# Kernel tuning notes

Hardware: AMD Instinct MI355X
Metric: run time of the kernel (lower is better)

The kernel has to match this reference:

```python
import jax, jax.numpy as jnp
import numpy as np

ALPHA = 0.85  # position gain (init kwarg alpha)
BETA = 0.005  # velocity gain (init kwarg beta)


def setup_inputs() -> dict:
    key = jax.random.key(0)
    Z = jax.random.normal(key, (4096, 8192), dtype=jnp.float32)
    return {"Z": Z}


def reference(Z) -> jnp.ndarray:
    # alpha-beta (g-h) filter recurrence, scanned over the time axis.
    #   diff = z - p;  x = p + a*diff;  v += b*diff;  p = x + v
    # Initial state: p = Z[:, 0], v = 0  (so x_0 == Z[:, 0]).
    a = jnp.asarray(ALPHA, Z.dtype)
    b = jnp.asarray(BETA, Z.dtype)

    def step(carry, z):
        p, v = carry
        diff = z - p
        x = p + a * diff
        v = v + b * diff
        p = x + v
        return (p, v), x

    p0 = Z[:, 0]
    v0 = jnp.zeros_like(p0)
    # scan over time: Z.T has shape [T, B]
    _, xs = jax.lax.scan(step, (p0, v0), Z.T)
    return xs.T  # [B, T]
```

## Files before the change

kernel.cpp:

```cpp
#include <hip/hip_runtime.h>


#define A_CONST 0.85f
#define B_CONST 0.005f

typedef float vfloat4 __attribute__((ext_vector_type(4)));

constexpr int ROWS   = 4096;
constexpr int T      = 8192;
constexpr int W      = 2048;
constexpr int L      = 32;
constexpr int NSEC   = T / W;
constexpr int STRIDE = 33;

__global__ __launch_bounds__(64)
void kalman_kernel(const float* __restrict__ Z, float* __restrict__ X) {
    const int lane = threadIdx.x;
    const int row  = blockIdx.x;

    __shared__ float buf[64 * STRIDE];

    const float* Zr = Z + (size_t)row * T;
    float*       Xr = X + (size_t)row * T;

    double a00 = 1.0 - (double)A_CONST - (double)B_CONST, a01 = 1.0;
    double a10 = -(double)B_CONST,                        a11 = 1.0;
    #pragma unroll
    for (int i = 0; i < 5; ++i) {
        double n00 = a00*a00 + a01*a10;
        double n01 = a00*a01 + a01*a11;
        double n10 = a10*a00 + a11*a10;
        double n11 = a10*a01 + a11*a11;
        a00 = n00; a01 = n01; a10 = n10; a11 = n11;
    }
    const float A32_00 = (float)a00, A32_01 = (float)a01;
    const float A32_10 = (float)a10, A32_11 = (float)a11;

    float ps = Zr[0];
    float vs = 0.0f;

    float4 r[8];
    {
        const float4* src = (const float4*)Zr;
        #pragma unroll
        for (int i = 0; i < 8; ++i) r[i] = src[i * 64 + lane];
    }

    for (int sec = 0; sec < NSEC; ++sec) {
        #pragma unroll
        for (int i = 0; i < 8; ++i) {
            int f = i * 64 + lane;
            int c = f >> 3;
            int j = (f & 7) << 2;
            float* p = buf + c * STRIDE + j;
            p[0] = r[i].x; p[1] = r[i].y; p[2] = r[i].z; p[3] = r[i].w;
        }

        if (sec + 1 < NSEC) {
            const float4* src = (const float4*)(Zr + (sec + 1) * W);
            #pragma unroll
            for (int i = 0; i < 8; ++i) r[i] = src[i * 64 + lane];
        }

        __syncthreads();

        float c32[L];
        float bp, bv;
        {
            float p = 0.0f, v = 0.0f;
            const float* zc = buf + lane * STRIDE;
            #pragma unroll
            for (int j = 0; j < L; ++j) {
                float z    = zc[j];
                c32[j]     = z;
                float diff = z - p;
                float x    = p + A_CONST * diff;
                v += B_CONST * diff;
                p  = x + v;
            }
            bp = p; bv = v;
        }

        float sA00 = A32_00, sA01 = A32_01, sA10 = A32_10, sA11 = A32_11;
        float sb0 = bp, sb1 = bv;
        #pragma unroll
        for (int d = 1; d < 64; d <<= 1) {
            float oA00 = __shfl_up(sA00, d);
            float oA01 = __shfl_up(sA01, d);
            float oA10 = __shfl_up(sA10, d);
            float oA11 = __shfl_up(sA11, d);
            float ob0  = __shfl_up(sb0,  d);
            float ob1  = __shfl_up(sb1,  d);
            if (lane >= d) {
                float n00 = sA00*oA00 + sA01*oA10;
                float n01 = sA00*oA01 + sA01*oA11;
                float n10 = sA10*oA00 + sA11*oA10;
                float n11 = sA10*oA01 + sA11*oA11;
                float nb0 = sA00*ob0 + sA01*ob1 + sb0;
                float nb1 = sA10*ob0 + sA11*ob1 + sb1;
                sA00 = n00; sA01 = n01; sA10 = n10; sA11 = n11;
                sb0 = nb0; sb1 = nb1;
            }
        }

        float eA00 = __shfl_up(sA00, 1);
        float eA01 = __shfl_up(sA01, 1);
        float eA10 = __shfl_up(sA10, 1);
        float eA11 = __shfl_up(sA11, 1);
        float eb0  = __shfl_up(sb0,  1);
        float eb1  = __shfl_up(sb1,  1);
        if (lane == 0) { eA00 = 1.f; eA01 = 0.f; eA10 = 0.f; eA11 = 1.f; eb0 = 0.f; eb1 = 0.f; }

        float iA00 = __shfl(sA00, 63);
        float iA01 = __shfl(sA01, 63);
        float iA10 = __shfl(sA10, 63);
        float iA11 = __shfl(sA11, 63);
        float ib0  = __shfl(sb0,  63);
        float ib1  = __shfl(sb1,  63);

        {
            float p = eA00*ps + eA01*vs + eb0;
            float v = eA10*ps + eA11*vs + eb1;
            float* zc = buf + lane * STRIDE;
            #pragma unroll
            for (int j = 0; j < L; ++j) {
                float z    = c32[j];
                float diff = z - p;
                float x    = p + A_CONST * diff;
                v += B_CONST * diff;
                p  = x + v;
                zc[j] = x;
            }
        }

        {
            float np = iA00*ps + iA01*vs + ib0;
            float nv = iA10*ps + iA11*vs + ib1;
            ps = np; vs = nv;
        }

        __syncthreads();

        {
            vfloat4* dst = (vfloat4*)(Xr + sec * W);
            #pragma unroll
            for (int i = 0; i < 8; ++i) {
                int f = i * 64 + lane;
                int c = f >> 3;
                int j = (f & 7) << 2;
                const float* p = buf + c * STRIDE + j;
                vfloat4 v4 = { p[0], p[1], p[2], p[3] };
                __builtin_nontemporal_store(v4, dst + f);
            }
        }

        __syncthreads();
    }
}

extern "C" void kernel_launch(void* const* d_in, const int* in_sizes, int n_in,
                              void* d_out, int out_size, void* d_ws, size_t ws_size,
                              hipStream_t stream) {
    const float* Z = (const float*)d_in[0];
    float*       X = (float*)d_out;
    dim3 grid(ROWS), block(64);
    hipLaunchKernelGGL(kalman_kernel, grid, block, 0, stream, Z, X);
}
```

Measured before the change: 45.58 us.

## Split each row's time axis into two halves with warm-up recurrence

Each row is now handled by two wavefronts, each covering half of the time axis. The second half starts 2048 samples early from a guessed state (p = z, v = 0) and runs warm-up sections without writing output. This relies on the filter's decaying state transition to converge to the true state. Section width drops to 1024 and blocks hold two waves, so the chunked scan keeps a shorter dependency chain per wave. In exchange it reads extra input for the warm-up, adds more barriers, and leaves a small approximation error at the split point.

Result: slower. 76.61 us (+68.1%).

```diff
diff --git a/kernel.cpp b/kernel.cpp
--- a/kernel.cpp
+++ b/kernel.cpp
@@ -6,65 +6,77 @@
 
 typedef float vfloat4 __attribute__((ext_vector_type(4)));
 
-constexpr int ROWS   = 4096;
-constexpr int T      = 8192;
-constexpr int W      = 2048;
-constexpr int L      = 32;
-constexpr int NSEC   = T / W;
-constexpr int STRIDE = 33;
+constexpr int ROWS      = 4096;
+constexpr int T         = 8192;
+constexpr int W         = 1024;
+constexpr int L         = 16;
+constexpr int STRIDE    = 17;
+constexpr int HALF      = T / 2;
+constexpr int NSEC_REAL = HALF / W;
+constexpr int WARM      = 2;
 
-__global__ __launch_bounds__(64)
+__global__ __launch_bounds__(128, 8)
 void kalman_kernel(const float* __restrict__ Z, float* __restrict__ X) {
-    const int lane = threadIdx.x;
-    const int row  = blockIdx.x;
+    const int wid  = threadIdx.x >> 6;
+    const int lane = threadIdx.x & 63;
+    const int g    = blockIdx.x * 2 + wid;
+    const int half = g >> 12;
+    const int row  = g & (ROWS - 1);
 
-    __shared__ float buf[64 * STRIDE];
+    __shared__ float lds[2][64 * STRIDE];
+    float* buf = lds[wid];
 
     const float* Zr = Z + (size_t)row * T;
     float*       Xr = X + (size_t)row * T;
 
+    const int nWarm = half ? WARM : 0;
+    const int nSec  = nWarm + NSEC_REAL;
+    const int start = half ? (HALF - WARM * W) : 0;
+    const float* Zs = Zr + start;
+    float*       Xs = Xr + start;
+
     double a00 = 1.0 - (double)A_CONST - (double)B_CONST, a01 = 1.0;
     double a10 = -(double)B_CONST,                        a11 = 1.0;
     #pragma unroll
-    for (int i = 0; i < 5; ++i) {
+    for (int i = 0; i < 4; ++i) {
         double n00 = a00*a00 + a01*a10;
         double n01 = a00*a01 + a01*a11;
         double n10 = a10*a00 + a11*a10;
         double n11 = a10*a01 + a11*a11;
         a00 = n00; a01 = n01; a10 = n10; a11 = n11;
     }
-    const float A32_00 = (float)a00, A32_01 = (float)a01;
-    const float A32_10 = (float)a10, A32_11 = (float)a11;
+    const float A16_00 = (float)a00, A16_01 = (float)a01;
+    const float A16_10 = (float)a10, A16_11 = (float)a11;
 
-    float ps = Zr[0];
+    float ps = Zs[0];
     float vs = 0.0f;
 
-    float4 r[8];
+    float4 r[4];
     {
-        const float4* src = (const float4*)Zr;
+        const float4* src = (const float4*)Zs;
         #pragma unroll
-        for (int i = 0; i < 8; ++i) r[i] = src[i * 64 + lane];
+        for (int i = 0; i < 4; ++i) r[i] = src[i * 64 + lane];
     }
 
-    for (int sec = 0; sec < NSEC; ++sec) {
+    for (int s = 0; s < nSec; ++s) {
         #pragma unroll
-        for (int i = 0; i < 8; ++i) {
+        for (int i = 0; i < 4; ++i) {
             int f = i * 64 + lane;
-            int c = f >> 3;
-            int j = (f & 7) << 2;
+            int c = f >> 2;
+            int j = (f & 3) << 2;
             float* p = buf + c * STRIDE + j;
             p[0] = r[i].x; p[1] = r[i].y; p[2] = r[i].z; p[3] = r[i].w;
         }
 
-        if (sec + 1 < NSEC) {
-            const float4* src = (const float4*)(Zr + (sec + 1) * W);
+        if (s + 1 < nSec) {
+            const float4* src = (const float4*)(Zs + (s + 1) * W);
             #pragma unroll
-            for (int i = 0; i < 8; ++i) r[i] = src[i * 64 + lane];
+            for (int i = 0; i < 4; ++i) r[i] = src[i * 64 + lane];
         }
 
         __syncthreads();
 
-        float c32[L];
+        float c16[L];
         float bp, bv;
         {
             float p = 0.0f, v = 0.0f;
@@ -72,7 +84,7 @@
             #pragma unroll
             for (int j = 0; j < L; ++j) {
                 float z    = zc[j];
-                c32[j]     = z;
+                c16[j]     = z;
                 float diff = z - p;
                 float x    = p + A_CONST * diff;
                 v += B_CONST * diff;
@@ -81,7 +93,7 @@
             bp = p; bv = v;
         }
 
-        float sA00 = A32_00, sA01 = A32_01, sA10 = A32_10, sA11 = A32_11;
+        float sA00 = A16_00, sA01 = A16_01, sA10 = A16_10, sA11 = A16_11;
         float sb0 = bp, sb1 = bv;
         #pragma unroll
         for (int d = 1; d < 64; d <<= 1) {
@@ -118,13 +130,13 @@
         float ib0  = __shfl(sb0,  63);
         float ib1  = __shfl(sb1,  63);
 
-        {
+        if (s >= nWarm) {
             float p = eA00*ps + eA01*vs + eb0;
             float v = eA10*ps + eA11*vs + eb1;
             float* zc = buf + lane * STRIDE;
             #pragma unroll
             for (int j = 0; j < L; ++j) {
-                float z    = c32[j];
+                float z    = c16[j];
                 float diff = z - p;
                 float x    = p + A_CONST * diff;
                 v += B_CONST * diff;
@@ -141,20 +153,19 @@
 
         __syncthreads();
 
-        {
-            vfloat4* dst = (vfloat4*)(Xr + sec * W);
+        if (s >= nWarm) {
+            vfloat4* dst = (vfloat4*)(Xs + s * W);
             #pragma unroll
-            for (int i = 0; i < 8; ++i) {
+            for (int i = 0; i < 4; ++i) {
                 int f = i * 64 + lane;
-                int c = f >> 3;
-                int j = (f & 7) << 2;
+                int c = f >> 2;
+                int j = (f & 3) << 2;
                 const float* p = buf + c * STRIDE + j;
                 vfloat4 v4 = { p[0], p[1], p[2], p[3] };
                 __builtin_nontemporal_store(v4, dst + f);
             }
+            __syncthreads();
         }
-
-        __syncthreads();
     }
 }
 
@@ -163,6 +174,6 @@
                               hipStream_t stream) {
     const float* Z = (const float*)d_in[0];
     float*       X = (float*)d_out;
-    dim3 grid(ROWS), block(64);
+    dim3 grid(ROWS), block(128);
     hipLaunchKernelGGL(kalman_kernel, grid, block, 0, stream, Z, X);
 }
```

## Use two waves per row with precomputed transition powers in the scan

Applied to the files above, without the earlier changes.

Each block now uses two wavefronts (128 threads) to process 4096-element sections, so there are two sections per row instead of four. The prefix scan no longer carries the 2x2 transition matrices through the shuffles. The power matrices A^(32·2^k) and each lane's exclusive prefix matrix are precomputed in double, leaving only two shuffles per scan step. The two waves combine their totals through a small shared scratch array and an extra barrier. This adds a block-level sync per section and more registers for the constant tables, in exchange for fewer shuffles and loop iterations.

Result: no change. 45.26 us (-0.7%).

```diff
diff --git a/kernel.cpp b/kernel.cpp
--- a/kernel.cpp
+++ b/kernel.cpp
@@ -8,33 +8,61 @@
 
 constexpr int ROWS   = 4096;
 constexpr int T      = 8192;
-constexpr int W      = 2048;
+constexpr int W      = 4096;
 constexpr int L      = 32;
 constexpr int NSEC   = T / W;
 constexpr int STRIDE = 33;
+constexpr int NCHUNK = W / L;
 
-__global__ __launch_bounds__(64)
+__global__ __launch_bounds__(128, 4)
 void kalman_kernel(const float* __restrict__ Z, float* __restrict__ X) {
-    const int lane = threadIdx.x;
+    const int tid  = threadIdx.x;
+    const int wid  = tid >> 6;
+    const int lane = tid & 63;
     const int row  = blockIdx.x;
 
-    __shared__ float buf[64 * STRIDE];
+    __shared__ float buf[NCHUNK * STRIDE];
+    __shared__ float scr[4];
 
     const float* Zr = Z + (size_t)row * T;
     float*       Xr = X + (size_t)row * T;
 
-    double a00 = 1.0 - (double)A_CONST - (double)B_CONST, a01 = 1.0;
-    double a10 = -(double)B_CONST,                        a11 = 1.0;
+    double m00 = 1.0 - (double)A_CONST - (double)B_CONST, m01 = 1.0;
+    double m10 = -(double)B_CONST,                        m11 = 1.0;
     #pragma unroll
     for (int i = 0; i < 5; ++i) {
-        double n00 = a00*a00 + a01*a10;
-        double n01 = a00*a01 + a01*a11;
-        double n10 = a10*a00 + a11*a10;
-        double n11 = a10*a01 + a11*a11;
-        a00 = n00; a01 = n01; a10 = n10; a11 = n11;
+        double n00 = m00*m00 + m01*m10, n01 = m00*m01 + m01*m11;
+        double n10 = m10*m00 + m11*m10, n11 = m10*m01 + m11*m11;
+        m00 = n00; m01 = n01; m10 = n10; m11 = n11;
     }
-    const float A32_00 = (float)a00, A32_01 = (float)a01;
-    const float A32_10 = (float)a10, A32_11 = (float)a11;
+    double g00[7], g01[7], g10[7], g11[7];
+    g00[0] = m00; g01[0] = m01; g10[0] = m10; g11[0] = m11;
+    #pragma unroll
+    for (int k = 1; k < 7; ++k) {
+        g00[k] = g00[k-1]*g00[k-1] + g01[k-1]*g10[k-1];
+        g01[k] = g00[k-1]*g01[k-1] + g01[k-1]*g11[k-1];
+        g10[k] = g10[k-1]*g00[k-1] + g11[k-1]*g10[k-1];
+        g11[k] = g10[k-1]*g01[k-1] + g11[k-1]*g11[k-1];
+    }
+    float sc00[6], sc01[6], sc10[6], sc11[6];
+    #pragma unroll
+    for (int k = 0; k < 6; ++k) {
+        sc00[k] = (float)g00[k]; sc01[k] = (float)g01[k];
+        sc10[k] = (float)g10[k]; sc11[k] = (float)g11[k];
+    }
+    const float w00 = (float)g00[6], w01 = (float)g01[6];
+    const float w10 = (float)g10[6], w11 = (float)g11[6];
+    double l00 = 1.0, l01 = 0.0, l10 = 0.0, l11 = 1.0;
+    #pragma unroll
+    for (int k = 0; k < 6; ++k) {
+        if ((lane >> k) & 1) {
+            double n00 = g00[k]*l00 + g01[k]*l10, n01 = g00[k]*l01 + g01[k]*l11;
+            double n10 = g10[k]*l00 + g11[k]*l10, n11 = g10[k]*l01 + g11[k]*l11;
+            l00 = n00; l01 = n01; l10 = n10; l11 = n11;
+        }
+    }
+    const float La00 = (float)l00, La01 = (float)l01;
+    const float La10 = (float)l10, La11 = (float)l11;
 
     float ps = Zr[0];
     float vs = 0.0f;
@@ -43,23 +71,23 @@
     {
         const float4* src = (const float4*)Zr;
         #pragma unroll
-        for (int i = 0; i < 8; ++i) r[i] = src[i * 64 + lane];
+        for (int i = 0; i < 8; ++i) r[i] = src[i * 128 + tid];
     }
 
-    for (int sec = 0; sec < NSEC; ++sec) {
+    for (int s = 0; s < NSEC; ++s) {
         #pragma unroll
         for (int i = 0; i < 8; ++i) {
-            int f = i * 64 + lane;
+            int f = i * 128 + tid;
             int c = f >> 3;
             int j = (f & 7) << 2;
             float* p = buf + c * STRIDE + j;
             p[0] = r[i].x; p[1] = r[i].y; p[2] = r[i].z; p[3] = r[i].w;
         }
 
-        if (sec + 1 < NSEC) {
-            const float4* src = (const float4*)(Zr + (sec + 1) * W);
+        if (s + 1 < NSEC) {
+            const float4* src = (const float4*)(Zr + (s + 1) * W);
             #pragma unroll
-            for (int i = 0; i < 8; ++i) r[i] = src[i * 64 + lane];
+            for (int i = 0; i < 8; ++i) r[i] = src[i * 128 + tid];
         }
 
         __syncthreads();
@@ -68,7 +96,7 @@
         float bp, bv;
         {
             float p = 0.0f, v = 0.0f;
-            const float* zc = buf + lane * STRIDE;
+            const float* zc = buf + tid * STRIDE;
             #pragma unroll
             for (int j = 0; j < L; ++j) {
                 float z    = zc[j];
@@ -81,47 +109,42 @@
             bp = p; bv = v;
         }
 
-        float sA00 = A32_00, sA01 = A32_01, sA10 = A32_10, sA11 = A32_11;
         float sb0 = bp, sb1 = bv;
         #pragma unroll
-        for (int d = 1; d < 64; d <<= 1) {
-            float oA00 = __shfl_up(sA00, d);
-            float oA01 = __shfl_up(sA01, d);
-            float oA10 = __shfl_up(sA10, d);
-            float oA11 = __shfl_up(sA11, d);
-            float ob0  = __shfl_up(sb0,  d);
-            float ob1  = __shfl_up(sb1,  d);
+        for (int k = 0; k < 6; ++k) {
+            const int d = 1 << k;
+            float ob0 = __shfl_up(sb0, d);
+            float ob1 = __shfl_up(sb1, d);
             if (lane >= d) {
-                float n00 = sA00*oA00 + sA01*oA10;
-                float n01 = sA00*oA01 + sA01*oA11;
-                float n10 = sA10*oA00 + sA11*oA10;
-                float n11 = sA10*oA01 + sA11*oA11;
-                float nb0 = sA00*ob0 + sA01*ob1 + sb0;
-                float nb1 = sA10*ob0 + sA11*ob1 + sb1;
-                sA00 = n00; sA01 = n01; sA10 = n10; sA11 = n11;
-                sb0 = nb0; sb1 = nb1;
+                sb0 = sc00[k]*ob0 + sc01[k]*ob1 + sb0;
+                sb1 = sc10[k]*ob0 + sc11[k]*ob1 + sb1;
             }
         }
 
-        float eA00 = __shfl_up(sA00, 1);
-        float eA01 = __shfl_up(sA01, 1);
-        float eA10 = __shfl_up(sA10, 1);
-        float eA11 = __shfl_up(sA11, 1);
-        float eb0  = __shfl_up(sb0,  1);
-        float eb1  = __shfl_up(sb1,  1);
-        if (lane == 0) { eA00 = 1.f; eA01 = 0.f; eA10 = 0.f; eA11 = 1.f; eb0 = 0.f; eb1 = 0.f; }
+        float eb0 = __shfl_up(sb0, 1);
+        float eb1 = __shfl_up(sb1, 1);
+        if (lane == 0) { eb0 = 0.0f; eb1 = 0.0f; }
 
-        float iA00 = __shfl(sA00, 63);
-        float iA01 = __shfl(sA01, 63);
-        float iA10 = __shfl(sA10, 63);
-        float iA11 = __shfl(sA11, 63);
-        float ib0  = __shfl(sb0,  63);
-        float ib1  = __shfl(sb1,  63);
+        float i0 = __shfl(sb0, 63);
+        float i1 = __shfl(sb1, 63);
+        if (lane == 0) { scr[wid * 2] = i0; scr[wid * 2 + 1] = i1; }
+        __syncthreads();
+
+        const float I00 = scr[0], I01 = scr[1];
+        const float I10 = scr[2], I11 = scr[3];
+
+        const float T0 = w00*ps + w01*vs + I00;
+        const float T1 = w10*ps + w11*vs + I01;
+        const float S0 = wid ? T0 : ps;
+        const float S1 = wid ? T1 : vs;
+        const float np = w00*T0 + w01*T1 + I10;
+        const float nv = w10*T0 + w11*T1 + I11;
+
+        float p = La00*S0 + La01*S1 + eb0;
+        float v = La10*S0 + La11*S1 + eb1;
 
         {
-            float p = eA00*ps + eA01*vs + eb0;
-            float v = eA10*ps + eA11*vs + eb1;
-            float* zc = buf + lane * STRIDE;
+            float* zc = buf + tid * STRIDE;
             #pragma unroll
             for (int j = 0; j < L; ++j) {
                 float z    = c32[j];
@@ -133,28 +156,24 @@
             }
         }
 
-        {
-            float np = iA00*ps + iA01*vs + ib0;
-            float nv = iA10*ps + iA11*vs + ib1;
-            ps = np; vs = nv;
-        }
-
         __syncthreads();
 
         {
-            vfloat4* dst = (vfloat4*)(Xr + sec * W);
+            vfloat4* dst = (vfloat4*)(Xr + s * W);
             #pragma unroll
             for (int i = 0; i < 8; ++i) {
-                int f = i * 64 + lane;
+                int f = i * 128 + tid;
                 int c = f >> 3;
                 int j = (f & 7) << 2;
-                const float* p = buf + c * STRIDE + j;
-                vfloat4 v4 = { p[0], p[1], p[2], p[3] };
+                const float* q = buf + c * STRIDE + j;
+                vfloat4 v4 = { q[0], q[1], q[2], q[3] };
                 __builtin_nontemporal_store(v4, dst + f);
             }
         }
 
         __syncthreads();
+
+        ps = np; vs = nv;
     }
 }
 
@@ -163,6 +182,6 @@
                               hipStream_t stream) {
     const float* Z = (const float*)d_in[0];
     float*       X = (float*)d_out;
-    dim3 grid(ROWS), block(64);
+    dim3 grid(ROWS), block(128);
     hipLaunchKernelGGL(kalman_kernel, grid, block, 0, stream, Z, X);
 }
```
